# Kernel optimization log

Hardware: AMD Instinct MI355X
Metric: run time of the kernel (lower is better)

## Reference

```python
import jax, jax.numpy as jnp
import numpy as np

# ---- constants (from init_kwargs / Box defaults) ----
B, K, T = 32768, 256, 10
C_LIGHT, F0, DF = 3.0e8, 1.0e10, 3.0e4
D_EL = C_LIGHT / (2.0 * F0)            # half-wavelength spacing
SPATIAL = F0 * D_EL / C_LIGHT          # = 0.5
RANGE_C = 2.0 * DF / C_LIGHT           # = 2e-4
THETA_MIN, THETA_MAX = -60.0, 60.0
R_MIN, R_MAX = 0.0, 2000.0
BETA = 2.0
STEP_CLIP = 0.1
INIT_ALPHA, INIT_LAMBDA = 0.01, 0.001
ALPHA_MIN, ALPHA_MAX = 1e-6, 0.2
LAM_MIN, LAM_MAX = 1e-6, 1.0
EPS = 1e-6


def _atanh(y):
    return jnp.arctanh(jnp.clip(y, -1.0 + EPS, 1.0 - EPS))


def map_theta_r_to_u(theta_deg, r_m):
    mid = 0.5 * (THETA_MIN + THETA_MAX)
    half = 0.5 * (THETA_MAX - THETA_MIN)
    y = (theta_deg - mid) / half
    s = jnp.clip((r_m - R_MIN) / (R_MAX - R_MIN), EPS, 1.0 - EPS)
    u_r = _atanh(2.0 * s - 1.0)          # tanh r_box inverse
    return jnp.stack([_atanh(y), u_r], axis=-1)  # (B,2)


def map_u_to_theta_r(u):
    mid = 0.5 * (THETA_MIN + THETA_MAX)
    half = 0.5 * (THETA_MAX - THETA_MIN)
    theta = mid + half * jnp.tanh(u[:, 0])
    s = 0.5 * (jnp.tanh(u[:, 1]) + 1.0)
    r = R_MIN + (R_MAX - R_MIN) * s
    return theta, r


def steering(theta_deg, r_m):
    # FDA steering: phase_k = 2*pi*k*(0.5*sin(theta) - 2*df*r/c)
    k = jnp.arange(K, dtype=jnp.float32)
    th = theta_deg * (jnp.pi / 180.0)
    phase = (2.0 * jnp.pi) * k[None, :] * (
        SPATIAL * jnp.sin(th)[:, None] - RANGE_C * r_m[:, None])  # (B,K)
    inv_sqrt_k = 1.0 / np.sqrt(K)
    return jnp.cos(phase) * inv_sqrt_k, jnp.sin(phase) * inv_sqrt_k


def loglike_logistic(theta_deg, r_m, z_re, z_im):
    # 1-bit logistic log-likelihood, summed over array elements -> (B,)
    a_re, a_im = steering(theta_deg, r_m)
    ll = jax.nn.log_sigmoid(BETA * z_re * a_re) + jax.nn.log_sigmoid(BETA * z_im * a_im)
    return jnp.sum(ll, axis=-1)


def setup_inputs() -> dict:
    key = jax.random.key(0)
    k1, k2, k3, k4 = jax.random.split(key, 4)
    z_real = jnp.sign(jax.random.normal(k1, (B, K), dtype=jnp.float32))
    z_imag = jnp.sign(jax.random.normal(k2, (B, K), dtype=jnp.float32))
    theta0 = jax.random.uniform(k3, (B,), jnp.float32, -55.0, 55.0)
    r0 = jax.random.uniform(k4, (B,), jnp.float32, 100.0, 1900.0)
    a_raw0 = float(np.log(np.expm1(INIT_ALPHA)))   # inverse softplus
    l_raw0 = float(np.log(np.expm1(INIT_LAMBDA)))
    return {
        "z_real": z_real, "z_imag": z_imag,
        "theta0_deg": theta0, "r0_m": r0,
        "alpha_theta_raw": jnp.full((T,), a_raw0, jnp.float32),
        "alpha_r_raw": jnp.full((T,), a_raw0, jnp.float32),
        "lambda_theta_raw": jnp.full((T,), l_raw0, jnp.float32),
        "lambda_r_raw": jnp.full((T,), l_raw0, jnp.float32),
    }


def reference(z_real, z_imag, theta0_deg, r0_m,
              alpha_theta_raw, alpha_r_raw, lambda_theta_raw, lambda_r_raw):
    alpha_th = jnp.clip(jax.nn.softplus(alpha_theta_raw), ALPHA_MIN, ALPHA_MAX)
    alpha_r = jnp.clip(jax.nn.softplus(alpha_r_raw), ALPHA_MIN, ALPHA_MAX)
    lam_th = jnp.clip(jax.nn.softplus(lambda_theta_raw), LAM_MIN, LAM_MAX)
    lam_r = jnp.clip(jax.nn.softplus(lambda_r_raw), LAM_MIN, LAM_MAX)

    u0 = map_theta_r_to_u(theta0_deg, r0_m)  # (B,2)

    def neg_obj_sum(u):
        th, r = map_u_to_theta_r(u)
        return -jnp.sum(loglike_logistic(th, r, z_real, z_imag))

    grad_fn = jax.grad(neg_obj_sum)

    def body(u, params):
        a_th, a_r, l_th, l_r = params
        # first-order unroll: gradient is a constant w.r.t. outer autodiff
        g = jax.lax.stop_gradient(grad_fn(u))
        g = jnp.where(jnp.isfinite(g), g, 0.0)
        g_th, g_r = g[:, 0], g[:, 1]
        a_th = jnp.where(jnp.isfinite(a_th), a_th, INIT_ALPHA)
        a_r = jnp.where(jnp.isfinite(a_r), a_r, INIT_ALPHA)
        l_th = jnp.where(jnp.isfinite(l_th), l_th, INIT_LAMBDA)
        l_r = jnp.where(jnp.isfinite(l_r), l_r, INIT_LAMBDA)
        den_th = jnp.maximum(jnp.nan_to_num(
            jnp.maximum(jnp.abs(g_th), 1e-6) + l_th, nan=1.0, posinf=1.0, neginf=1.0), 1e-6)
        den_r = jnp.maximum(jnp.nan_to_num(
            jnp.maximum(jnp.abs(g_r), 1e-6) + l_r, nan=1.0, posinf=1.0, neginf=1.0), 1e-6)
        step_u = jnp.stack([a_th * g_th / den_th, a_r * g_r / den_r], axis=-1)
        step_u = jnp.clip(jnp.nan_to_num(step_u, nan=0.0, posinf=0.0, neginf=0.0),
                          -STEP_CLIP, STEP_CLIP)
        return u - step_u, None

    uT, _ = jax.lax.scan(body, u0, (alpha_th, alpha_r, lam_th, lam_r))
    theta_T, r_T = map_u_to_theta_r(uT)
    return jnp.stack([theta_T, r_T], axis=-1)  # (B,2)
```

## Files before the change

kernel.cpp:

```cpp
#include <hip/hip_runtime.h>
#include <cstdint>

#define PI_F 3.14159265358979323846f

__device__ __forceinline__ float fract_(float x)  { return __builtin_amdgcn_fractf(x); }
__device__ __forceinline__ float sin2pi_(float r) { return __builtin_amdgcn_sinf(r); }
__device__ __forceinline__ float cos2pi_(float r) { return __builtin_amdgcn_cosf(r); }

extern "C" __global__ void __launch_bounds__(256)
pack_signs(const float4* __restrict__ zr, const float4* __restrict__ zi,
           uint32_t* __restrict__ pr, uint32_t* __restrict__ pim) {
    const int t = blockIdx.x * 256 + threadIdx.x;
    uint32_t wr = 0u, wi = 0u;
    #pragma unroll
    for (int q = 0; q < 8; ++q) {
        const float4 a = zr[t * 8 + q];
        const float4 b = zi[t * 8 + q];
        wr |= ((uint32_t)(a.x < 0.f) << (4 * q))     | ((uint32_t)(a.y < 0.f) << (4 * q + 1))
            | ((uint32_t)(a.z < 0.f) << (4 * q + 2)) | ((uint32_t)(a.w < 0.f) << (4 * q + 3));
        wi |= ((uint32_t)(b.x < 0.f) << (4 * q))     | ((uint32_t)(b.y < 0.f) << (4 * q + 1))
            | ((uint32_t)(b.z < 0.f) << (4 * q + 2)) | ((uint32_t)(b.w < 0.f) << (4 * q + 3));
    }
    pr[t] = wr;
    pim[t] = wi;
}

extern "C" __global__ void __launch_bounds__(256)
refine(const float* __restrict__ th0, const float* __restrict__ r0,
       const float* __restrict__ a_th_raw, const float* __restrict__ a_r_raw,
       const float* __restrict__ l_th_raw, const float* __restrict__ l_r_raw,
       const uint32_t* __restrict__ pr, const uint32_t* __restrict__ pim,
       float* __restrict__ out) {
    const int lane = threadIdx.x & 63;
    const int w    = threadIdx.x >> 6;
    const int item = blockIdx.x * 64 + lane;

    __shared__ float sp[4][10];
    __shared__ float red[2][4][64];

    if (threadIdx.x < 40) {
        const int a = threadIdx.x / 10, i = threadIdx.x % 10;
        const float* src = (a == 0) ? a_th_raw : (a == 1) ? a_r_raw
                         : (a == 2) ? l_th_raw : l_r_raw;
        const float v  = log1pf(expf(src[i]));
        const float hi = (a < 2) ? 0.2f : 1.0f;
        sp[a][i] = fminf(fmaxf(v, 1e-6f), hi);
    }

    const uint32_t br0 = pr [item * 8 + w * 2 + 0];
    const uint32_t br1 = pr [item * 8 + w * 2 + 1];
    const uint32_t bi0 = pim[item * 8 + w * 2 + 0];
    const uint32_t bi1 = pim[item * 8 + w * 2 + 1];

    float y = th0[item] * (1.0f / 60.0f);
    y = fminf(fmaxf(y, -1.0f + 1e-6f), 1.0f - 1e-6f);
    float u0 = atanhf(y);
    float sR = r0[item] * (1.0f / 2000.0f);
    sR = fminf(fmaxf(sR, 1e-6f), 1.0f - 1e-6f);
    float u1 = atanhf(2.0f * sR - 1.0f);

    const float w64 = (float)(w * 64);

    __syncthreads();

    for (int t = 0; t < 10; ++t) {
        const float ath = sp[0][t], ar = sp[1][t], lth = sp[2][t], lr = sp[3][t];

        const float T0 = tanhf(u0), T1 = tanhf(u1);
        const float th_rad = (PI_F / 3.0f) * T0;
        const float sth = sinf(th_rad), cth = cosf(th_rad);
        const float r   = 1000.0f * (T1 + 1.0f);
        const float crev = 0.5f * sth - 2e-4f * r;

        const float d4 = fract_(4.0f * crev);
        const float C4 = cos2pi_(d4), S4 = sin2pi_(d4);

        float c[4], s[4], kf[4], acc[4];
        #pragma unroll
        for (int m = 0; m < 4; ++m) {
            const float k0 = w64 + (float)m;
            const float rv = fract_(k0 * crev);
            c[m] = cos2pi_(rv);
            s[m] = sin2pi_(rv);
            kf[m]  = k0;
            acc[m] = 0.0f;
        }

        #pragma unroll
        for (int j = 0; j < 16; ++j) {
            #pragma unroll
            for (int m = 0; m < 4; ++m) {
                const int kl = m + 4 * j;
                const uint32_t wr = (kl < 32) ? br0 : br1;
                const uint32_t wi = (kl < 32) ? bi0 : bi1;
                const int sh = 31 - (kl & 31);
                const uint32_t mre = (wr << sh) & 0x80000000u;
                const uint32_t mim = (wi << sh) & 0x80000000u;
                const float cs = c[m], ss = s[m];
                const float zc = __uint_as_float(__float_as_uint(cs) ^ mim);
                const float zs = __uint_as_float(__float_as_uint(ss) ^ mre);
                const float w0 = zc - zs;
                const float u2 = ss * ss;
                const float t2 = fmaf(-2.0f, u2, 1.0f);
                const float sc = ss * cs;
                const float v  = sc * t2;
                const float W  = fmaf(v, -(1.0f / 196608.0f), w0 * 0.0625f);
                acc[m] = fmaf(kf[m], W, acc[m]);
                kf[m] += 4.0f;
                const float tA = ss * S4;
                const float tB = cs * S4;
                c[m] = fmaf(cs, C4, -tA);
                s[m] = fmaf(ss, C4, tB);
            }
        }
        float S = (acc[0] + acc[1]) + (acc[2] + acc[3]);

        const int p = t & 1;
        red[p][w][lane] = S;
        __syncthreads();
        S = (red[p][0][lane] + red[p][1][lane]) + (red[p][2][lane] + red[p][3][lane]);

        const float g0 = -(PI_F * PI_F / 3.0f) * cth * (1.0f - T0 * T0) * S;
        const float g1 = 0.4f * PI_F * (1.0f - T1 * T1) * S;
        const float den0 = fmaxf(fabsf(g0), 1e-6f) + lth;
        const float den1 = fmaxf(fabsf(g1), 1e-6f) + lr;
        float st0 = ath * g0 / den0;
        float st1 = ar  * g1 / den1;
        st0 = fminf(fmaxf(st0, -0.1f), 0.1f);
        st1 = fminf(fmaxf(st1, -0.1f), 0.1f);
        u0 -= st0;
        u1 -= st1;
    }

    if (w == 0) {
        const float thT = 60.0f * tanhf(u0);
        const float rT  = 1000.0f * (tanhf(u1) + 1.0f);
        reinterpret_cast<float2*>(out)[item] = make_float2(thT, rT);
    }
}

extern "C" void kernel_launch(void* const* d_in, const int* in_sizes, int n_in,
                              void* d_out, int out_size, void* d_ws, size_t ws_size,
                              hipStream_t stream) {
    const float* zr   = (const float*)d_in[0];
    const float* zi   = (const float*)d_in[1];
    const float* th0  = (const float*)d_in[2];
    const float* r0   = (const float*)d_in[3];
    const float* athr = (const float*)d_in[4];
    const float* arr  = (const float*)d_in[5];
    const float* lthr = (const float*)d_in[6];
    const float* lrr  = (const float*)d_in[7];

    const int B  = in_sizes[2];
    const int BK = in_sizes[0];

    uint32_t* pr  = (uint32_t*)d_ws;
    uint32_t* pim = pr + (size_t)B * 8;

    pack_signs<<<(BK / 32) / 256, 256, 0, stream>>>((const float4*)zr, (const float4*)zi,
                                                    pr, pim);
    refine<<<B / 64, 256, 0, stream>>>(th0, r0, athr, arr, lthr, lrr, pr, pim,
                                       (float*)d_out);
}
```

Baseline: 139.1 us.

## Split each wavefront across two items with 128-thread blocks of 32 items

Refine blocks shrink from 256 threads handling 64 items to 128 threads handling 32 items. Each 64-lane wavefront now covers two K-groups for 32 items instead of one K-group for 64 items. This gives twice as many smaller blocks, which may help load balance and occupancy across CUs. The 1/16 scale is also moved out of the inner loop and applied once to the partial sum. The cost is more per-item scalar work, since the tanh and sin math runs on 4 lanes per item, and the pack-array reads become less coalesced.

```diff
diff --git a/kernel.cpp b/kernel.cpp
--- a/kernel.cpp
+++ b/kernel.cpp
@@ -25,21 +25,24 @@
     pim[t] = wi;
 }
 
-extern "C" __global__ void __launch_bounds__(256)
+extern "C" __global__ void __launch_bounds__(128, 4)
 refine(const float* __restrict__ th0, const float* __restrict__ r0,
        const float* __restrict__ a_th_raw, const float* __restrict__ a_r_raw,
        const float* __restrict__ l_th_raw, const float* __restrict__ l_r_raw,
        const uint32_t* __restrict__ pr, const uint32_t* __restrict__ pim,
        float* __restrict__ out) {
-    const int lane = threadIdx.x & 63;
-    const int w    = threadIdx.x >> 6;
-    const int item = blockIdx.x * 64 + lane;
+    const int tid  = threadIdx.x;
+    const int lane = tid & 63;
+    const int wv   = tid >> 6;
+    const int it   = lane & 31;
+    const int g    = 2 * wv + (lane >> 5);
+    const int item = blockIdx.x * 32 + it;
 
     __shared__ float sp[4][10];
-    __shared__ float red[2][4][64];
+    __shared__ float red[2][4][32];
 
-    if (threadIdx.x < 40) {
-        const int a = threadIdx.x / 10, i = threadIdx.x % 10;
+    if (tid < 40) {
+        const int a = tid / 10, i = tid % 10;
         const float* src = (a == 0) ? a_th_raw : (a == 1) ? a_r_raw
                          : (a == 2) ? l_th_raw : l_r_raw;
         const float v  = log1pf(expf(src[i]));
@@ -47,10 +50,10 @@
         sp[a][i] = fminf(fmaxf(v, 1e-6f), hi);
     }
 
-    const uint32_t br0 = pr [item * 8 + w * 2 + 0];
-    const uint32_t br1 = pr [item * 8 + w * 2 + 1];
-    const uint32_t bi0 = pim[item * 8 + w * 2 + 0];
-    const uint32_t bi1 = pim[item * 8 + w * 2 + 1];
+    const uint32_t br0 = pr [item * 8 + g * 2 + 0];
+    const uint32_t br1 = pr [item * 8 + g * 2 + 1];
+    const uint32_t bi0 = pim[item * 8 + g * 2 + 0];
+    const uint32_t bi1 = pim[item * 8 + g * 2 + 1];
 
     float y = th0[item] * (1.0f / 60.0f);
     y = fminf(fmaxf(y, -1.0f + 1e-6f), 1.0f - 1e-6f);
@@ -59,7 +62,7 @@
     sR = fminf(fmaxf(sR, 1e-6f), 1.0f - 1e-6f);
     float u1 = atanhf(2.0f * sR - 1.0f);
 
-    const float w64 = (float)(w * 64);
+    const float w64 = (float)(g * 64);
 
     __syncthreads();
 
@@ -104,8 +107,8 @@
                 const float t2 = fmaf(-2.0f, u2, 1.0f);
                 const float sc = ss * cs;
                 const float v  = sc * t2;
-                const float W  = fmaf(v, -(1.0f / 196608.0f), w0 * 0.0625f);
-                acc[m] = fmaf(kf[m], W, acc[m]);
+                const float W16 = fmaf(v, -(16.0f / 196608.0f), w0);
+                acc[m] = fmaf(kf[m], W16, acc[m]);
                 kf[m] += 4.0f;
                 const float tA = ss * S4;
                 const float tB = cs * S4;
@@ -113,12 +116,14 @@
                 s[m] = fmaf(ss, C4, tB);
             }
         }
-        float S = (acc[0] + acc[1]) + (acc[2] + acc[3]);
+        const float partial = ((acc[0] + acc[1]) + (acc[2] + acc[3])) * 0.0625f;
 
         const int p = t & 1;
-        red[p][w][lane] = S;
+        red[p][g][it] = partial;
         __syncthreads();
-        S = (red[p][0][lane] + red[p][1][lane]) + (red[p][2][lane] + red[p][3][lane]);
+
+        const float S = (red[p][0][it] + red[p][1][it])
+                      + (red[p][2][it] + red[p][3][it]);
 
         const float g0 = -(PI_F * PI_F / 3.0f) * cth * (1.0f - T0 * T0) * S;
         const float g1 = 0.4f * PI_F * (1.0f - T1 * T1) * S;
@@ -132,7 +137,7 @@
         u1 -= st1;
     }
 
-    if (w == 0) {
+    if (tid < 32) {
         const float thT = 60.0f * tanhf(u0);
         const float rT  = 1000.0f * (tanhf(u1) + 1.0f);
         reinterpret_cast<float2*>(out)[item] = make_float2(thT, rT);
@@ -159,6 +164,6 @@
 
     pack_signs<<<(BK / 32) / 256, 256, 0, stream>>>((const float4*)zr, (const float4*)zi,
                                                     pr, pim);
-    refine<<<B / 64, 256, 0, stream>>>(th0, r0, athr, arr, lthr, lrr, pr, pim,
+    refine<<<B / 32, 128, 0, stream>>>(th0, r0, athr, arr, lthr, lrr, pr, pim,
                                        (float*)d_out);
 }
```

Result: slower. 318.5 us (+129.0%).
